# Performance work log

Measured on AMD Instinct MI355X. Metric: run time of the kernel, lower is better.

Reference implementation:

```python
import jax, jax.numpy as jnp
import numpy as np

B, Q, D, C, N = 4, 100, 128, 20, 262144
LN_EPS = 1e-5


def setup_inputs() -> dict:
    key = jax.random.key(0)
    ks = jax.random.split(key, 8)
    s = 1.0 / np.sqrt(D).astype(np.float32)
    return {
        "query_feat": jax.random.normal(ks[0], (B, Q, D), jnp.float32),
        "point_feats": jax.random.normal(ks[1], (N, D), jnp.float32),
        "batch_ids": jnp.sort(jax.random.randint(ks[2], (N,), 0, B, dtype=jnp.int32)),
        "ln_gamma": jnp.ones((D,), jnp.float32),
        "ln_beta": jnp.zeros((D,), jnp.float32),
        "W1": jax.random.normal(ks[3], (D, D), jnp.float32) * s,
        "b1": jnp.zeros((D,), jnp.float32),
        "W2": jax.random.normal(ks[4], (D, D), jnp.float32) * s,
        "b2": jnp.zeros((D,), jnp.float32),
        "Wc": jax.random.normal(ks[5], (C, D), jnp.float32) * s,
        "bc": jnp.zeros((C,), jnp.float32),
    }


def reference(query_feat, point_feats, batch_ids, ln_gamma, ln_beta, W1, b1, W2, b2, Wc, bc):
    # decoder_norm: LayerNorm over hidden dim
    mu = jnp.mean(query_feat, axis=-1, keepdims=True)
    var = jnp.var(query_feat, axis=-1, keepdims=True)
    qn = (query_feat - mu) * jax.lax.rsqrt(var + LN_EPS) * ln_gamma + ln_beta  # [B,Q,D]

    # mask_embed_head: Linear -> ReLU -> Linear (torch Linear: x @ W.T + b)
    h = jax.nn.relu(jnp.einsum('bqd,ed->bqe', qn, W1) + b1)
    mask_embed = jnp.einsum('bqd,ed->bqe', h, W2) + b2  # [B,Q,D]

    # class_embed_head
    outputs_class = jnp.einsum('bqd,cd->bqc', qn, Wc) + bc  # [B,Q,C]

    # Ragged per-batch matmul: for each point n, point_feats[n] @ mask_embed[batch_ids[n]].T.
    # Equivalent to the original concat of decomposed_features[i] @ mask_embed[i].T
    # because batch_ids is sorted. Loop is over the small fixed batch count only.
    nb = mask_embed.shape[0]
    out_masks = jnp.zeros((point_feats.shape[0], mask_embed.shape[1]), point_feats.dtype)
    for b in range(nb):
        sel = (batch_ids == b)[:, None]
        out_masks = out_masks + jnp.where(sel, point_feats @ mask_embed[b].T, 0.0)
    return outputs_class, out_masks
```

## Files before the change

### kernel.cpp

```cpp
#include <hip/hip_runtime.h>
#include <hip/hip_bf16.h>

typedef __bf16 bf16x8 __attribute__((ext_vector_type(8)));
typedef float f32x4 __attribute__((ext_vector_type(4)));
typedef unsigned short ushort8 __attribute__((ext_vector_type(8)));

#define B_    4
#define Q_    100
#define QPAD  112
#define D_    128
#define C_    20
#define N_    262144
#define TN    256
#define LROW  136
#define LN_EPS 1e-5f

__global__ __launch_bounds__(128) void head_kernel(
    const float* __restrict__ qf,
    const float* __restrict__ gamma, const float* __restrict__ beta,
    const float* __restrict__ W1, const float* __restrict__ b1,
    const float* __restrict__ W2, const float* __restrict__ b2,
    const float* __restrict__ Wc, const float* __restrict__ bc,
    float* __restrict__ out_class,
    unsigned short* __restrict__ me_hi, unsigned short* __restrict__ me_lo)
{
    const int q = blockIdx.x;
    const int b = blockIdx.y;
    const int t = threadIdx.x;

    unsigned short* mh = me_hi + (b * QPAD + q) * D_;
    unsigned short* ml = me_lo + (b * QPAD + q) * D_;
    if (q >= Q_) { mh[t] = 0; ml[t] = 0; return; }

    __shared__ float red[D_];
    __shared__ float qs[D_];
    __shared__ float hs[D_];

    const float x = qf[(b * Q_ + q) * D_ + t];

    red[t] = x;
    __syncthreads();
    #pragma unroll
    for (int s = 64; s > 0; s >>= 1) { if (t < s) red[t] += red[t + s]; __syncthreads(); }
    const float mu = red[0] * (1.0f / 128.0f);
    __syncthreads();
    const float xc = x - mu;
    red[t] = xc * xc;
    __syncthreads();
    #pragma unroll
    for (int s = 64; s > 0; s >>= 1) { if (t < s) red[t] += red[t + s]; __syncthreads(); }
    const float var = red[0] * (1.0f / 128.0f);

    const float xn = xc * rsqrtf(var + LN_EPS) * gamma[t] + beta[t];
    qs[t] = xn;
    __syncthreads();

    {
        const float4* wr = (const float4*)(W1 + t * D_);
        float p0 = 0.f, p1 = 0.f, p2 = 0.f, p3 = 0.f;
        #pragma unroll
        for (int d4 = 0; d4 < 32; ++d4) {
            const float4 w = wr[d4];
            const int d = d4 * 4;
            p0 = fmaf(w.x, qs[d + 0], p0);
            p1 = fmaf(w.y, qs[d + 1], p1);
            p2 = fmaf(w.z, qs[d + 2], p2);
            p3 = fmaf(w.w, qs[d + 3], p3);
        }
        hs[t] = fmaxf((p0 + p1) + (p2 + p3) + b1[t], 0.0f);
    }
    __syncthreads();

    {
        const float4* wr = (const float4*)(W2 + t * D_);
        float p0 = 0.f, p1 = 0.f, p2 = 0.f, p3 = 0.f;
        #pragma unroll
        for (int d4 = 0; d4 < 32; ++d4) {
            const float4 w = wr[d4];
            const int d = d4 * 4;
            p0 = fmaf(w.x, hs[d + 0], p0);
            p1 = fmaf(w.y, hs[d + 1], p1);
            p2 = fmaf(w.z, hs[d + 2], p2);
            p3 = fmaf(w.w, hs[d + 3], p3);
        }
        const float me = (p0 + p1) + (p2 + p3) + b2[t];
        const __bf16 hi = (__bf16)me;
        const __bf16 lo = (__bf16)(me - (float)hi);
        mh[t] = __builtin_bit_cast(unsigned short, hi);
        ml[t] = __builtin_bit_cast(unsigned short, lo);
    }

    if (t < C_) {
        const float4* wr = (const float4*)(Wc + t * D_);
        float p0 = 0.f, p1 = 0.f, p2 = 0.f, p3 = 0.f;
        #pragma unroll
        for (int d4 = 0; d4 < 32; ++d4) {
            const float4 w = wr[d4];
            const int d = d4 * 4;
            p0 = fmaf(w.x, qs[d + 0], p0);
            p1 = fmaf(w.y, qs[d + 1], p1);
            p2 = fmaf(w.z, qs[d + 2], p2);
            p3 = fmaf(w.w, qs[d + 3], p3);
        }
        out_class[(b * Q_ + q) * C_ + t] = (p0 + p1) + (p2 + p3) + bc[t];
    }
}

__global__ __launch_bounds__(1024, 8) void mask_kernel(
    const float* __restrict__ points, const int* __restrict__ bids,
    const unsigned short* __restrict__ me_hi, const unsigned short* __restrict__ me_lo,
    float* __restrict__ outm)
{
    const int n0 = blockIdx.x * TN;

    __shared__ unsigned short BH[QPAD][LROW];
    __shared__ unsigned short BL[QPAD][LROW];
    __shared__ int sbid[TN];

    const int tid = threadIdx.x;
    if (tid < TN) sbid[tid] = bids[n0 + tid];

    const int b_lo = bids[n0];
    const int b_hi = bids[n0 + TN - 1];

    const int wave = tid >> 6;
    const int lane = tid & 63;
    const int ar   = lane & 15;
    const int kg   = lane >> 4;
    const int qlane = lane & 15;

    long nout[4];
    int  prow_id[4];
    #pragma unroll
    for (int rr = 0; rr < 4; ++rr) {
        const int pl = wave * 16 + kg * 4 + rr;
        prow_id[rr] = pl;
        nout[rr] = (long)(n0 + pl) * Q_;
    }

    for (int b = b_lo; b <= b_hi; ++b) {
        if (b != b_lo) __syncthreads();

        {
            const ushort8* sh = (const ushort8*)(me_hi + b * QPAD * D_);
            const ushort8* sl = (const ushort8*)(me_lo + b * QPAD * D_);
            for (int c = tid; c < QPAD * D_ / 8; c += 1024) {
                const int row = c >> 4;
                const int col = c & 15;
                *(ushort8*)&BH[row][col * 8] = sh[c];
                *(ushort8*)&BL[row][col * 8] = sl[c];
            }
        }
        __syncthreads();

        const float* prow = points + (size_t)(n0 + wave * 16 + ar) * D_;
        bf16x8 AH[4], AL[4];
        #pragma unroll
        for (int kt = 0; kt < 4; ++kt) {
            const int k0 = kt * 32 + kg * 8;
            const float4 f0 = *(const float4*)(prow + k0);
            const float4 f1 = *(const float4*)(prow + k0 + 4);
            const float fv0[4] = {f0.x, f0.y, f0.z, f0.w};
            const float fv1[4] = {f1.x, f1.y, f1.z, f1.w};
            #pragma unroll
            for (int j = 0; j < 4; ++j) {
                const __bf16 h0 = (__bf16)fv0[j];
                AH[kt][j] = h0;
                AL[kt][j] = (__bf16)(fv0[j] - (float)h0);
                const __bf16 h1 = (__bf16)fv1[j];
                AH[kt][j + 4] = h1;
                AL[kt][j + 4] = (__bf16)(fv1[j] - (float)h1);
            }
        }

        bool act[4];
        #pragma unroll
        for (int rr = 0; rr < 4; ++rr) act[rr] = (sbid[prow_id[rr]] == b);

        #pragma unroll
        for (int qt = 0; qt < 7; ++qt) {
            f32x4 acc = {0.f, 0.f, 0.f, 0.f};
            const int qrow = qt * 16 + qlane;
            #pragma unroll
            for (int kt = 0; kt < 4; ++kt) {
                const int kb = kt * 32 + kg * 8;
                const bf16x8 bh = __builtin_bit_cast(bf16x8, *(const ushort8*)&BH[qrow][kb]);
                const bf16x8 bl = __builtin_bit_cast(bf16x8, *(const ushort8*)&BL[qrow][kb]);
                acc = __builtin_amdgcn_mfma_f32_16x16x32_bf16(AL[kt], bh, acc, 0, 0, 0);
                acc = __builtin_amdgcn_mfma_f32_16x16x32_bf16(AH[kt], bl, acc, 0, 0, 0);
                acc = __builtin_amdgcn_mfma_f32_16x16x32_bf16(AH[kt], bh, acc, 0, 0, 0);
            }
            if (qrow < Q_) {
                #pragma unroll
                for (int rr = 0; rr < 4; ++rr) {
                    if (act[rr]) outm[nout[rr] + qrow] = acc[rr];
                }
            }
        }
    }
}

extern "C" void kernel_launch(void* const* d_in, const int* in_sizes, int n_in,
                              void* d_out, int out_size, void* d_ws, size_t ws_size,
                              hipStream_t stream) {
    const float* qf    = (const float*)d_in[0];
    const float* pf    = (const float*)d_in[1];
    const int*   bids  = (const int*)  d_in[2];
    const float* gamma = (const float*)d_in[3];
    const float* beta  = (const float*)d_in[4];
    const float* W1    = (const float*)d_in[5];
    const float* b1    = (const float*)d_in[6];
    const float* W2    = (const float*)d_in[7];
    const float* b2    = (const float*)d_in[8];
    const float* Wc    = (const float*)d_in[9];
    const float* bc    = (const float*)d_in[10];

    float* out_class = (float*)d_out;
    float* out_masks = out_class + B_ * Q_ * C_;

    unsigned short* me_hi = (unsigned short*)d_ws;
    unsigned short* me_lo = me_hi + B_ * QPAD * D_;

    head_kernel<<<dim3(QPAD, B_), 128, 0, stream>>>(
        qf, gamma, beta, W1, b1, W2, b2, Wc, bc, out_class, me_hi, me_lo);

    mask_kernel<<<dim3(N_ / TN), 1024, 0, stream>>>(
        pf, bids, me_hi, me_lo, out_masks);
}
```

Measured before the change: 282.2 us.

## Drop LDS staging of mask embeddings; two row tiles per wave with direct global loads

The mask kernel no longer stages the hi/lo bf16 mask embeddings in shared memory. Each wave loads its B fragments straight from global memory (L1/L2 cached) and reuses them across two 16-row point tiles, so every wave covers 32 points. Blocks shrink from 1024 to 256 threads with no barriers, per-row batch ids are read from global, and output writes become nontemporal stores. The aim is to remove LDS fill and barrier costs and raise B-fragment reuse, at the price of more global/L2 traffic for the embeddings and more registers per thread.

```diff
diff --git a/kernel.cpp b/kernel.cpp
--- a/kernel.cpp
+++ b/kernel.cpp
@@ -11,8 +11,7 @@
 #define D_    128
 #define C_    20
 #define N_    262144
-#define TN    256
-#define LROW  136
+#define TN    128
 #define LN_EPS 1e-5f
 
 __global__ __launch_bounds__(128) void head_kernel(
@@ -106,55 +105,25 @@
     }
 }
 
-__global__ __launch_bounds__(1024, 8) void mask_kernel(
+__global__ __launch_bounds__(256) void mask_kernel(
     const float* __restrict__ points, const int* __restrict__ bids,
     const unsigned short* __restrict__ me_hi, const unsigned short* __restrict__ me_lo,
     float* __restrict__ outm)
 {
-    const int n0 = blockIdx.x * TN;
-
-    __shared__ unsigned short BH[QPAD][LROW];
-    __shared__ unsigned short BL[QPAD][LROW];
-    __shared__ int sbid[TN];
-
-    const int tid = threadIdx.x;
-    if (tid < TN) sbid[tid] = bids[n0 + tid];
-
-    const int b_lo = bids[n0];
-    const int b_hi = bids[n0 + TN - 1];
-
+    const int n0   = blockIdx.x * TN;
+    const int tid  = threadIdx.x;
     const int wave = tid >> 6;
     const int lane = tid & 63;
     const int ar   = lane & 15;
     const int kg   = lane >> 4;
     const int qlane = lane & 15;
 
-    long nout[4];
-    int  prow_id[4];
-    #pragma unroll
-    for (int rr = 0; rr < 4; ++rr) {
-        const int pl = wave * 16 + kg * 4 + rr;
-        prow_id[rr] = pl;
-        nout[rr] = (long)(n0 + pl) * Q_;
-    }
-
-    for (int b = b_lo; b <= b_hi; ++b) {
-        if (b != b_lo) __syncthreads();
-
-        {
-            const ushort8* sh = (const ushort8*)(me_hi + b * QPAD * D_);
-            const ushort8* sl = (const ushort8*)(me_lo + b * QPAD * D_);
-            for (int c = tid; c < QPAD * D_ / 8; c += 1024) {
-                const int row = c >> 4;
-                const int col = c & 15;
-                *(ushort8*)&BH[row][col * 8] = sh[c];
-                *(ushort8*)&BL[row][col * 8] = sl[c];
-            }
-        }
-        __syncthreads();
-
-        const float* prow = points + (size_t)(n0 + wave * 16 + ar) * D_;
-        bf16x8 AH[4], AL[4];
+    const int r0 = n0 + wave * 32;
+
+    bf16x8 AH[2][4], AL[2][4];
+    #pragma unroll
+    for (int s = 0; s < 2; ++s) {
+        const float* prow = points + (size_t)(r0 + s * 16 + ar) * D_;
         #pragma unroll
         for (int kt = 0; kt < 4; ++kt) {
             const int k0 = kt * 32 + kg * 8;
@@ -165,35 +134,64 @@
             #pragma unroll
             for (int j = 0; j < 4; ++j) {
                 const __bf16 h0 = (__bf16)fv0[j];
-                AH[kt][j] = h0;
-                AL[kt][j] = (__bf16)(fv0[j] - (float)h0);
+                AH[s][kt][j] = h0;
+                AL[s][kt][j] = (__bf16)(fv0[j] - (float)h0);
                 const __bf16 h1 = (__bf16)fv1[j];
-                AH[kt][j + 4] = h1;
-                AL[kt][j + 4] = (__bf16)(fv1[j] - (float)h1);
-            }
-        }
-
-        bool act[4];
-        #pragma unroll
-        for (int rr = 0; rr < 4; ++rr) act[rr] = (sbid[prow_id[rr]] == b);
+                AH[s][kt][j + 4] = h1;
+                AL[s][kt][j + 4] = (__bf16)(fv1[j] - (float)h1);
+            }
+        }
+    }
+
+    const int b_lo = bids[n0];
+    const int b_hi = bids[n0 + TN - 1];
+    int  myb[2][4];
+    long nout[2][4];
+    #pragma unroll
+    for (int s = 0; s < 2; ++s) {
+        #pragma unroll
+        for (int rr = 0; rr < 4; ++rr) {
+            const int row = r0 + s * 16 + kg * 4 + rr;
+            myb[s][rr]  = bids[row];
+            nout[s][rr] = (long)row * Q_;
+        }
+    }
+
+    for (int b = b_lo; b <= b_hi; ++b) {
+        const unsigned short* bh_base = me_hi + (size_t)b * QPAD * D_;
+        const unsigned short* bl_base = me_lo + (size_t)b * QPAD * D_;
 
         #pragma unroll
         for (int qt = 0; qt < 7; ++qt) {
-            f32x4 acc = {0.f, 0.f, 0.f, 0.f};
             const int qrow = qt * 16 + qlane;
+            const int qoff = qrow * D_ + kg * 8;
+
+            bf16x8 bh[4], bl[4];
             #pragma unroll
             for (int kt = 0; kt < 4; ++kt) {
-                const int kb = kt * 32 + kg * 8;
-                const bf16x8 bh = __builtin_bit_cast(bf16x8, *(const ushort8*)&BH[qrow][kb]);
-                const bf16x8 bl = __builtin_bit_cast(bf16x8, *(const ushort8*)&BL[qrow][kb]);
-                acc = __builtin_amdgcn_mfma_f32_16x16x32_bf16(AL[kt], bh, acc, 0, 0, 0);
-                acc = __builtin_amdgcn_mfma_f32_16x16x32_bf16(AH[kt], bl, acc, 0, 0, 0);
-                acc = __builtin_amdgcn_mfma_f32_16x16x32_bf16(AH[kt], bh, acc, 0, 0, 0);
-            }
+                bh[kt] = __builtin_bit_cast(bf16x8, *(const ushort8*)(bh_base + qoff + kt * 32));
+                bl[kt] = __builtin_bit_cast(bf16x8, *(const ushort8*)(bl_base + qoff + kt * 32));
+            }
+
+            f32x4 acc0 = {0.f, 0.f, 0.f, 0.f};
+            f32x4 acc1 = {0.f, 0.f, 0.f, 0.f};
+            #pragma unroll
+            for (int kt = 0; kt < 4; ++kt) {
+                acc0 = __builtin_amdgcn_mfma_f32_16x16x32_bf16(AL[0][kt], bh[kt], acc0, 0, 0, 0);
+                acc1 = __builtin_amdgcn_mfma_f32_16x16x32_bf16(AL[1][kt], bh[kt], acc1, 0, 0, 0);
+                acc0 = __builtin_amdgcn_mfma_f32_16x16x32_bf16(AH[0][kt], bl[kt], acc0, 0, 0, 0);
+                acc1 = __builtin_amdgcn_mfma_f32_16x16x32_bf16(AH[1][kt], bl[kt], acc1, 0, 0, 0);
+                acc0 = __builtin_amdgcn_mfma_f32_16x16x32_bf16(AH[0][kt], bh[kt], acc0, 0, 0, 0);
+                acc1 = __builtin_amdgcn_mfma_f32_16x16x32_bf16(AH[1][kt], bh[kt], acc1, 0, 0, 0);
+            }
+
             if (qrow < Q_) {
                 #pragma unroll
                 for (int rr = 0; rr < 4; ++rr) {
-                    if (act[rr]) outm[nout[rr] + qrow] = acc[rr];
+                    if (myb[0][rr] == b)
+                        __builtin_nontemporal_store(acc0[rr], &outm[nout[0][rr] + qrow]);
+                    if (myb[1][rr] == b)
+                        __builtin_nontemporal_store(acc1[rr], &outm[nout[1][rr] + qrow]);
                 }
             }
         }
@@ -224,6 +222,6 @@
     head_kernel<<<dim3(QPAD, B_), 128, 0, stream>>>(
         qf, gamma, beta, W1, b1, W2, b2, Wc, bc, out_class, me_hi, me_lo);
 
-    mask_kernel<<<dim3(N_ / TN), 1024, 0, stream>>>(
+    mask_kernel<<<dim3(N_ / TN), 256, 0, stream>>>(
         pf, bids, me_hi, me_lo, out_masks);
 }
```

Result: slower. 342.0 us (+21.2%).

## Process two point chunks per block with register prefetch and cached mask-embed staging

Applied to the files above, without the earlier changes.

Each block now handles two 256-point chunks. It prefetches the next chunk's point rows into registers while converting the current chunk to split bf16, and it only restages the mask-embed tile in LDS when the batch id changes. Per-row batch ids are read straight from global memory instead of an LDS copy, and launch bounds drop to 4 blocks per CU. This is meant to hide global load latency and amortise the LDS staging, at the cost of more registers and half as many blocks.

```diff
diff --git a/kernel.cpp b/kernel.cpp
--- a/kernel.cpp
+++ b/kernel.cpp
@@ -12,6 +12,7 @@
 #define C_    20
 #define N_    262144
 #define TN    256
+#define CPB   2
 #define LROW  136
 #define LN_EPS 1e-5f
 
@@ -106,94 +107,107 @@
     }
 }
 
-__global__ __launch_bounds__(1024, 8) void mask_kernel(
+__global__ __launch_bounds__(1024, 4) void mask_kernel(
     const float* __restrict__ points, const int* __restrict__ bids,
     const unsigned short* __restrict__ me_hi, const unsigned short* __restrict__ me_lo,
     float* __restrict__ outm)
 {
-    const int n0 = blockIdx.x * TN;
-
-    __shared__ unsigned short BH[QPAD][LROW];
-    __shared__ unsigned short BL[QPAD][LROW];
-    __shared__ int sbid[TN];
-
-    const int tid = threadIdx.x;
-    if (tid < TN) sbid[tid] = bids[n0 + tid];
-
-    const int b_lo = bids[n0];
-    const int b_hi = bids[n0 + TN - 1];
-
+    const int tid  = threadIdx.x;
     const int wave = tid >> 6;
     const int lane = tid & 63;
     const int ar   = lane & 15;
     const int kg   = lane >> 4;
     const int qlane = lane & 15;
 
-    long nout[4];
-    int  prow_id[4];
-    #pragma unroll
-    for (int rr = 0; rr < 4; ++rr) {
-        const int pl = wave * 16 + kg * 4 + rr;
-        prow_id[rr] = pl;
-        nout[rr] = (long)(n0 + pl) * Q_;
-    }
-
-    for (int b = b_lo; b <= b_hi; ++b) {
-        if (b != b_lo) __syncthreads();
-
-        {
-            const ushort8* sh = (const ushort8*)(me_hi + b * QPAD * D_);
-            const ushort8* sl = (const ushort8*)(me_lo + b * QPAD * D_);
-            for (int c = tid; c < QPAD * D_ / 8; c += 1024) {
-                const int row = c >> 4;
-                const int col = c & 15;
-                *(ushort8*)&BH[row][col * 8] = sh[c];
-                *(ushort8*)&BL[row][col * 8] = sl[c];
-            }
-        }
-        __syncthreads();
-
-        const float* prow = points + (size_t)(n0 + wave * 16 + ar) * D_;
+    __shared__ unsigned short BH[QPAD][LROW];
+    __shared__ unsigned short BL[QPAD][LROW];
+
+    int staged_b = -1;
+    const int base = blockIdx.x * (TN * CPB);
+
+    float4 fv[8];
+    {
+        const float* prow = points + (size_t)(base + wave * 16 + ar) * D_;
+        #pragma unroll
+        for (int kt = 0; kt < 4; ++kt) {
+            fv[2 * kt]     = *(const float4*)(prow + kt * 32 + kg * 8);
+            fv[2 * kt + 1] = *(const float4*)(prow + kt * 32 + kg * 8 + 4);
+        }
+    }
+
+    for (int k = 0; k < CPB; ++k) {
+        const int n0 = base + k * TN;
+
         bf16x8 AH[4], AL[4];
         #pragma unroll
         for (int kt = 0; kt < 4; ++kt) {
-            const int k0 = kt * 32 + kg * 8;
-            const float4 f0 = *(const float4*)(prow + k0);
-            const float4 f1 = *(const float4*)(prow + k0 + 4);
-            const float fv0[4] = {f0.x, f0.y, f0.z, f0.w};
-            const float fv1[4] = {f1.x, f1.y, f1.z, f1.w};
+            const float f0[4] = {fv[2*kt].x, fv[2*kt].y, fv[2*kt].z, fv[2*kt].w};
+            const float f1[4] = {fv[2*kt+1].x, fv[2*kt+1].y, fv[2*kt+1].z, fv[2*kt+1].w};
             #pragma unroll
             for (int j = 0; j < 4; ++j) {
-                const __bf16 h0 = (__bf16)fv0[j];
+                const __bf16 h0 = (__bf16)f0[j];
                 AH[kt][j] = h0;
-                AL[kt][j] = (__bf16)(fv0[j] - (float)h0);
-                const __bf16 h1 = (__bf16)fv1[j];
+                AL[kt][j] = (__bf16)(f0[j] - (float)h0);
+                const __bf16 h1 = (__bf16)f1[j];
                 AH[kt][j + 4] = h1;
-                AL[kt][j + 4] = (__bf16)(fv1[j] - (float)h1);
-            }
-        }
-
-        bool act[4];
-        #pragma unroll
-        for (int rr = 0; rr < 4; ++rr) act[rr] = (sbid[prow_id[rr]] == b);
-
-        #pragma unroll
-        for (int qt = 0; qt < 7; ++qt) {
-            f32x4 acc = {0.f, 0.f, 0.f, 0.f};
-            const int qrow = qt * 16 + qlane;
+                AL[kt][j + 4] = (__bf16)(f1[j] - (float)h1);
+            }
+        }
+
+        if (k + 1 < CPB) {
+            const float* prow = points + (size_t)(n0 + TN + wave * 16 + ar) * D_;
             #pragma unroll
             for (int kt = 0; kt < 4; ++kt) {
-                const int kb = kt * 32 + kg * 8;
-                const bf16x8 bh = __builtin_bit_cast(bf16x8, *(const ushort8*)&BH[qrow][kb]);
-                const bf16x8 bl = __builtin_bit_cast(bf16x8, *(const ushort8*)&BL[qrow][kb]);
-                acc = __builtin_amdgcn_mfma_f32_16x16x32_bf16(AL[kt], bh, acc, 0, 0, 0);
-                acc = __builtin_amdgcn_mfma_f32_16x16x32_bf16(AH[kt], bl, acc, 0, 0, 0);
-                acc = __builtin_amdgcn_mfma_f32_16x16x32_bf16(AH[kt], bh, acc, 0, 0, 0);
-            }
-            if (qrow < Q_) {
+                fv[2 * kt]     = *(const float4*)(prow + kt * 32 + kg * 8);
+                fv[2 * kt + 1] = *(const float4*)(prow + kt * 32 + kg * 8 + 4);
+            }
+        }
+
+        int  myb[4];
+        long nout[4];
+        #pragma unroll
+        for (int rr = 0; rr < 4; ++rr) {
+            const int row = n0 + wave * 16 + kg * 4 + rr;
+            myb[rr]  = bids[row];
+            nout[rr] = (long)row * Q_;
+        }
+
+        const int b_lo = bids[n0];
+        const int b_hi = bids[n0 + TN - 1];
+
+        for (int b = b_lo; b <= b_hi; ++b) {
+            if (b != staged_b) {
+                __syncthreads();
+                const ushort8* sh = (const ushort8*)(me_hi + (size_t)b * QPAD * D_);
+                const ushort8* sl = (const ushort8*)(me_lo + (size_t)b * QPAD * D_);
+                for (int c = tid; c < QPAD * D_ / 8; c += 1024) {
+                    const int row = c >> 4;
+                    const int col = c & 15;
+                    *(ushort8*)&BH[row][col * 8] = sh[c];
+                    *(ushort8*)&BL[row][col * 8] = sl[c];
+                }
+                __syncthreads();
+                staged_b = b;
+            }
+
+            #pragma unroll
+            for (int qt = 0; qt < 7; ++qt) {
+                f32x4 acc = {0.f, 0.f, 0.f, 0.f};
+                const int qrow = qt * 16 + qlane;
                 #pragma unroll
-                for (int rr = 0; rr < 4; ++rr) {
-                    if (act[rr]) outm[nout[rr] + qrow] = acc[rr];
+                for (int kt = 0; kt < 4; ++kt) {
+                    const int kb = kt * 32 + kg * 8;
+                    const bf16x8 bh = __builtin_bit_cast(bf16x8, *(const ushort8*)&BH[qrow][kb]);
+                    const bf16x8 bl = __builtin_bit_cast(bf16x8, *(const ushort8*)&BL[qrow][kb]);
+                    acc = __builtin_amdgcn_mfma_f32_16x16x32_bf16(AL[kt], bh, acc, 0, 0, 0);
+                    acc = __builtin_amdgcn_mfma_f32_16x16x32_bf16(AH[kt], bl, acc, 0, 0, 0);
+                    acc = __builtin_amdgcn_mfma_f32_16x16x32_bf16(AH[kt], bh, acc, 0, 0, 0);
+                }
+                if (qrow < Q_) {
+                    #pragma unroll
+                    for (int rr = 0; rr < 4; ++rr) {
+                        if (myb[rr] == b) outm[nout[rr] + qrow] = acc[rr];
+                    }
                 }
             }
         }
@@ -224,6 +238,6 @@
     head_kernel<<<dim3(QPAD, B_), 128, 0, stream>>>(
         qf, gamma, beta, W1, b1, W2, b2, Wc, bc, out_class, me_hi, me_lo);
 
-    mask_kernel<<<dim3(N_ / TN), 1024, 0, stream>>>(
+    mask_kernel<<<dim3(N_ / (TN * CPB)), 1024, 0, stream>>>(
         pf, bids, me_hi, me_lo, out_masks);
 }
```

After: 282.4 us. About the same (+0.1%).
